# Kernel tuning notes

Hardware: AMD Instinct MI355X
Metric: run time of the kernel (lower is better)

The kernel has to match this reference:

```python
import jax, jax.numpy as jnp
import numpy as np

NEG_INF = -1000000.0  # matches the original's -1e6 masking constant


def setup_inputs() -> dict:
    key = jax.random.key(0)
    ks = jax.random.split(key, 7)
    B, S, A, Q, D = 32, 2048, 1024, 1024, 1024  # batch, src len, attend_dim, query_dim, att_dim
    return {
        "input": jax.random.normal(ks[0], (B, 1, Q), dtype=jnp.float32),
        "context": jax.random.normal(ks[1], (B, S, A), dtype=jnp.float32),
        "W_pre": jax.random.normal(ks[2], (D, A), dtype=jnp.float32) * 0.02,
        "b_pre": jax.random.normal(ks[3], (D,), dtype=jnp.float32) * 0.02,
        "W_q": jax.random.normal(ks[4], (D, Q), dtype=jnp.float32) * 0.02,
        "v": jax.random.normal(ks[5], (D,), dtype=jnp.float32) * 0.02,
        "mask": jax.random.randint(ks[6], (B, 1, S), 0, 2, dtype=jnp.int32),
    }


def reference(input, context, W_pre, b_pre, W_q, v, mask):
    # precompute = linear_pre(context): [B, S, D]
    precompute = jnp.einsum("bsa,da->bsd", context, W_pre) + b_pre
    # targetT = linear_q(input): [B, 1, D]; repeat over S via broadcast
    targetT = jnp.einsum("bqc,dc->bqd", input, W_q)
    tmp = jnp.tanh(precompute + targetT)                 # [B, S, D]
    energy = jnp.einsum("bsd,d->bs", tmp, v)             # linear_v -> [B, S]
    # mask: positions where mask == 0 get -1e6 (energy*(1-m) + m*(-1e6), m = (mask==0))
    masked_out = (mask[:, 0, :] == 0)
    energy = jnp.where(masked_out, NEG_INF, energy)
    score = jax.nn.softmax(energy, axis=1)               # softmax over S
    score_m = score[:, None, :]                          # [B, 1, S]
    weightedContext = jnp.einsum("bqs,bsa->bqa", score_m, context)  # [B, 1, A]
    return weightedContext, score_m, precompute
```

## Files before the change

kernel.cpp:

```cpp
#include <hip/hip_runtime.h>

#define NEG_INF_VAL -1000000.0f

typedef short s16x8 __attribute__((ext_vector_type(8)));
typedef float f32x4 __attribute__((ext_vector_type(4)));

__device__ __forceinline__ unsigned int bf16_rne(float f) {
  unsigned int u = __float_as_uint(f);
  return (u + 0x7fffu + ((u >> 16) & 1u)) >> 16;
}
__device__ __forceinline__ unsigned int pack_bf2(float a, float b) {
  return bf16_rne(a) | (bf16_rne(b) << 16);
}

__device__ __forceinline__ float fast_tanh(float x) {
  float t = __expf(2.f * x);
  return 1.f - __fdividef(2.f, t + 1.f);
}

__global__ __launch_bounds__(256) void convert_bf16_kernel(
    const float* __restrict__ src, unsigned short* __restrict__ dst, long n) {
  long i = ((long)blockIdx.x * blockDim.x + threadIdx.x) * 8;
  long stride = (long)gridDim.x * blockDim.x * 8;
  for (; i < n; i += stride) {
    float4 f0 = *(const float4*)(src + i);
    float4 f1 = *(const float4*)(src + i + 4);
    uint4 o;
    o.x = pack_bf2(f0.x, f0.y);
    o.y = pack_bf2(f0.z, f0.w);
    o.z = pack_bf2(f1.x, f1.y);
    o.w = pack_bf2(f1.z, f1.w);
    *(uint4*)(dst + i) = o;
  }
}

__global__ __launch_bounds__(256) void targetT_kernel(
    const float* __restrict__ input, const float* __restrict__ Wq,
    float* __restrict__ tT) {
  int d0 = blockIdx.x * 8;
  int t = threadIdx.x;
  int b = t >> 3, dl = t & 7;
  __shared__ float in_s[32][32];
  __shared__ float wq_s[8][32];
  float acc = 0.f;
  for (int q0 = 0; q0 < 1024; q0 += 32) {
    int r = t >> 3, c = (t & 7) * 4;
    *(float4*)&in_s[r][c] = *(const float4*)&input[r * 1024 + q0 + c];
    wq_s[t >> 5][t & 31] = Wq[(long)(d0 + (t >> 5)) * 1024 + q0 + (t & 31)];
    __syncthreads();
#pragma unroll
    for (int qq = 0; qq < 32; ++qq)
      acc += in_s[b][qq] * wq_s[dl][qq];
    __syncthreads();
  }
  tT[b * 1024 + d0 + dl] = acc;
}

__device__ __forceinline__ void load_lds16(const void* g, void* l) {
  __builtin_amdgcn_global_load_lds(
      (const __attribute__((address_space(1))) void*)g,
      (__attribute__((address_space(3))) void*)l, 16, 0, 0);
}

__global__ __launch_bounds__(256, 4) void gemm_energy_kernel(
    const unsigned short* __restrict__ A,
    const unsigned short* __restrict__ B,
    const float* __restrict__ b_pre,
    const float* __restrict__ tT,
    const float* __restrict__ vvec,
    float* __restrict__ Cout,
    float* __restrict__ epart) {
  const int K = 1024;
  const int N = 1024;
  int lin = blockIdx.x;
  int w = (lin & 7) * 512 + (lin >> 3);
  int nt = w & 7;
  int mt = w >> 3;
  int m0 = mt * 128, n0 = nt * 128;
  int tid = threadIdx.x;
  int lane = tid & 63, wid = tid >> 6;
  int wr = wid >> 1, wc = wid & 1;

  __shared__ unsigned short sA[128][32];
  __shared__ unsigned short sB[128][32];

  f32x4 acc[4][4] = {};

  int srow = lane >> 2;
  int scol = ((lane & 3) ^ ((lane >> 3) & 3)) * 8;
  const unsigned short* Ag = A + (long)(m0 + wid * 32 + srow) * K + scol;
  const unsigned short* Bg = B + (long)(n0 + wid * 32 + srow) * K + scol;
  unsigned short* sA0 = &sA[wid * 32][0];
  unsigned short* sA1 = &sA[wid * 32 + 16][0];
  unsigned short* sB0 = &sB[wid * 32][0];
  unsigned short* sB1 = &sB[wid * 32 + 16][0];

  int r = lane & 15, g = lane >> 4;
  int slotA = (g ^ ((r >> 1) & 3)) * 8;

  for (int k0 = 0; k0 < K; k0 += 32) {
    load_lds16(Ag, sA0);
    load_lds16(Ag + 16 * K, sA1);
    load_lds16(Bg, sB0);
    load_lds16(Bg + 16 * K, sB1);
    Ag += 32; Bg += 32;
    asm volatile("s_waitcnt vmcnt(0)" ::: "memory");
    __syncthreads();
    s16x8 af[4], bfr[4];
#pragma unroll
    for (int i = 0; i < 4; ++i)
      af[i] = *(const s16x8*)&sA[wr * 64 + i * 16 + r][slotA];
#pragma unroll
    for (int j = 0; j < 4; ++j)
      bfr[j] = *(const s16x8*)&sB[wc * 64 + j * 16 + r][slotA];
    __builtin_amdgcn_s_setprio(1);
#pragma unroll
    for (int i = 0; i < 4; ++i)
#pragma unroll
      for (int j = 0; j < 4; ++j)
        acc[i][j] = __builtin_amdgcn_mfma_f32_16x16x32_bf16(af[i], bfr[j], acc[i][j], 0, 0, 0);
    __builtin_amdgcn_s_setprio(0);
    __syncthreads();
  }

  int b = m0 >> 11;
  float bp[4], tv[4], vv[4];
#pragma unroll
  for (int j = 0; j < 4; ++j) {
    int d = n0 + wc * 64 + j * 16 + r;
    bp[j] = b_pre[d];
    tv[j] = tT[b * 1024 + d];
    vv[j] = vvec[d];
  }
#pragma unroll
  for (int i = 0; i < 4; ++i) {
#pragma unroll
    for (int q = 0; q < 4; ++q) {
      int m = m0 + wr * 64 + i * 16 + g * 4 + q;
      float e = 0.f;
#pragma unroll
      for (int j = 0; j < 4; ++j) {
        float val = acc[i][j][q] + bp[j];
        Cout[(long)m * N + n0 + wc * 64 + j * 16 + r] = val;
        e += fast_tanh(val + tv[j]) * vv[j];
      }
      e += __shfl_xor(e, 1);
      e += __shfl_xor(e, 2);
      e += __shfl_xor(e, 4);
      e += __shfl_xor(e, 8);
      if (r == 0) epart[(long)m * 16 + nt * 2 + wc] = e;
    }
  }
}

__global__ __launch_bounds__(256) void softmax_kernel(
    const float* __restrict__ epart, const int* __restrict__ mask,
    float* __restrict__ score) {
  int b = blockIdx.x;
  int t = threadIdx.x;
  __shared__ float red[256];
  float ev[8];
  float mx = -3.4e38f;
#pragma unroll
  for (int ii = 0; ii < 8; ++ii) {
    int s = ii * 256 + t;
    long m = (long)b * 2048 + s;
    const float4* p = (const float4*)(epart + m * 16);
    float4 p0 = p[0], p1 = p[1], p2 = p[2], p3 = p[3];
    float e = p0.x + p0.y + p0.z + p0.w + p1.x + p1.y + p1.z + p1.w
            + p2.x + p2.y + p2.z + p2.w + p3.x + p3.y + p3.z + p3.w;
    if (mask[b * 2048 + s] == 0) e = NEG_INF_VAL;
    ev[ii] = e;
    mx = fmaxf(mx, e);
  }
  red[t] = mx; __syncthreads();
  for (int off = 128; off > 0; off >>= 1) {
    if (t < off) red[t] = fmaxf(red[t], red[t + off]);
    __syncthreads();
  }
  mx = red[0];
  __syncthreads();
  float sum = 0.f;
#pragma unroll
  for (int ii = 0; ii < 8; ++ii) { ev[ii] = __expf(ev[ii] - mx); sum += ev[ii]; }
  red[t] = sum; __syncthreads();
  for (int off = 128; off > 0; off >>= 1) {
    if (t < off) red[t] += red[t + off];
    __syncthreads();
  }
  float inv = 1.f / red[0];
#pragma unroll
  for (int ii = 0; ii < 8; ++ii)
    score[b * 2048 + ii * 256 + t] = ev[ii] * inv;
}

__global__ __launch_bounds__(256) void wc_partial_kernel(
    const unsigned short* __restrict__ ctx, const float* __restrict__ score,
    float* __restrict__ part) {
  int b = blockIdx.x, sc = blockIdx.y;
  int t = threadIdx.x;
  __shared__ float ssc[64];
  if (t < 64) ssc[t] = score[b * 2048 + sc * 64 + t];
  __syncthreads();
  float acc0 = 0.f, acc1 = 0.f, acc2 = 0.f, acc3 = 0.f;
  const unsigned short* cp = ctx + ((long)b * 2048 + sc * 64) * 1024 + t * 4;
  for (int s = 0; s < 64; ++s) {
    uint2 pk = *(const uint2*)cp;
    cp += 1024;
    float wgt = ssc[s];
    acc0 += wgt * __uint_as_float(pk.x << 16);
    acc1 += wgt * __uint_as_float(pk.x & 0xffff0000u);
    acc2 += wgt * __uint_as_float(pk.y << 16);
    acc3 += wgt * __uint_as_float(pk.y & 0xffff0000u);
  }
  float* pp = part + ((long)(b * 32 + sc)) * 1024 + t * 4;
  pp[0] = acc0; pp[1] = acc1; pp[2] = acc2; pp[3] = acc3;
}

__global__ __launch_bounds__(256) void wc_reduce_kernel(
    const float* __restrict__ part, float* __restrict__ wc) {
  int id = blockIdx.x * 256 + threadIdx.x;
  int b = id >> 10, a = id & 1023;
  float s = 0.f;
#pragma unroll
  for (int scn = 0; scn < 32; ++scn)
    s += part[((long)(b * 32 + scn)) * 1024 + a];
  wc[id] = s;
}

extern "C" void kernel_launch(void* const* d_in, const int* in_sizes, int n_in,
                              void* d_out, int out_size, void* d_ws, size_t ws_size,
                              hipStream_t stream) {
  const float* input   = (const float*)d_in[0];
  const float* context = (const float*)d_in[1];
  const float* W_pre   = (const float*)d_in[2];
  const float* b_pre   = (const float*)d_in[3];
  const float* W_q     = (const float*)d_in[4];
  const float* v       = (const float*)d_in[5];
  const int*   mask    = (const int*)d_in[6];

  float* out       = (float*)d_out;
  float* out_wc    = out;
  float* out_score = out + 32768;
  float* out_pre   = out + 98304;

  const size_t OFF_CTX   = 0;
  const size_t OFF_WPRE  = 134217728;
  const size_t OFF_TT    = 136314880;
  const size_t OFF_EPART = 136445952;
  const size_t OFF_WCP   = 140640256;
  const size_t WS_NEED   = 144834560;
  if (ws_size < WS_NEED) return;

  char* ws = (char*)d_ws;
  unsigned short* ctx_bf  = (unsigned short*)(ws + OFF_CTX);
  unsigned short* wpre_bf = (unsigned short*)(ws + OFF_WPRE);
  float* tT     = (float*)(ws + OFF_TT);
  float* epart  = (float*)(ws + OFF_EPART);
  float* wcpart = (float*)(ws + OFF_WCP);

  convert_bf16_kernel<<<2048, 256, 0, stream>>>(context, ctx_bf, 64LL * 1024 * 1024);
  convert_bf16_kernel<<<256, 256, 0, stream>>>(W_pre, wpre_bf, 1024LL * 1024);
  targetT_kernel<<<128, 256, 0, stream>>>(input, W_q, tT);
  gemm_energy_kernel<<<4096, 256, 0, stream>>>(ctx_bf, wpre_bf, b_pre, tT, v,
                                               out_pre, epart);
  softmax_kernel<<<32, 256, 0, stream>>>(epart, mask, out_score);
  dim3 g5(32, 32);
  wc_partial_kernel<<<g5, 256, 0, stream>>>(ctx_bf, out_score, wcpart);
  wc_reduce_kernel<<<128, 256, 0, stream>>>(wcpart, out_wc);
}
```

Before: 364.7 us.

## Double-buffer GEMM LDS tiles with prefetch and one barrier per phase

Restructures the bf16 GEMM main loop into a software pipeline. Two LDS buffers are used: the tile for a future k-step is issued with global_load_lds while MFMAs run on the current one, and vmcnt is partially waited with a single s_barrier per phase. This replaces the old load, wait-all, sync, compute, sync sequence, which exposed global memory latency on every k-step. It doubles LDS use and lowers the launch-bounds occupancy hint from 4 to 2. The final iteration also prefetches a tile past the end of K that is never used, which reads slightly beyond the row and possibly beyond the buffer.

```diff
diff --git a/kernel.cpp b/kernel.cpp
--- a/kernel.cpp
+++ b/kernel.cpp
@@ -62,16 +62,55 @@
       (__attribute__((address_space(3))) void*)l, 16, 0, 0);
 }
 
-__global__ __launch_bounds__(256, 4) void gemm_energy_kernel(
+#define STAGE_AB(SB, SKK, SKT)                                                       \
+  {                                                                                  \
+    const unsigned short* gpA = Ag + (SKT) * 64 + (SKK) * 32;                        \
+    const unsigned short* gpB = Bg + (SKT) * 64 + (SKK) * 32;                        \
+    char* lpA = dstB + (SB) * 32768 + (SKK) * 8192;                                  \
+    load_lds16(gpA, lpA);                                                            \
+    load_lds16(gpA + 16 * 1024, lpA + 1024);                                         \
+    load_lds16(gpB, lpA + 16384);                                                    \
+    load_lds16(gpB + 16 * 1024, lpA + 16384 + 1024);                                 \
+  }
+
+#define MFMA_ROW(I, AF)                                                              \
+  acc[I][0] = __builtin_amdgcn_mfma_f32_16x16x32_bf16(AF, bf0, acc[I][0], 0, 0, 0);  \
+  acc[I][1] = __builtin_amdgcn_mfma_f32_16x16x32_bf16(AF, bf1, acc[I][1], 0, 0, 0);  \
+  acc[I][2] = __builtin_amdgcn_mfma_f32_16x16x32_bf16(AF, bf2, acc[I][2], 0, 0, 0);  \
+  acc[I][3] = __builtin_amdgcn_mfma_f32_16x16x32_bf16(AF, bf3, acc[I][3], 0, 0, 0);
+
+#define PHASE(BUF, KK, SB, SKT)                                                      \
+  {                                                                                  \
+    const unsigned short* pA = (BUF) ? pA1 : pA0;                                    \
+    const unsigned short* pB = (BUF) ? pB1 : pB0;                                    \
+    s16x8 af0 = *(const s16x8*)(pA + (KK)*4096 +    0);                              \
+    s16x8 af1 = *(const s16x8*)(pA + (KK)*4096 +  512);                              \
+    s16x8 af2 = *(const s16x8*)(pA + (KK)*4096 + 1024);                              \
+    s16x8 af3 = *(const s16x8*)(pA + (KK)*4096 + 1536);                              \
+    s16x8 bf0 = *(const s16x8*)(pB + (KK)*4096 +    0);                              \
+    s16x8 bf1 = *(const s16x8*)(pB + (KK)*4096 +  512);                              \
+    s16x8 bf2 = *(const s16x8*)(pB + (KK)*4096 + 1024);                              \
+    s16x8 bf3 = *(const s16x8*)(pB + (KK)*4096 + 1536);                              \
+    STAGE_AB(SB, KK, SKT)                                                            \
+    __builtin_amdgcn_s_setprio(1);                                                   \
+    MFMA_ROW(0, af0)                                                                 \
+    MFMA_ROW(1, af1)                                                                 \
+    MFMA_ROW(2, af2)                                                                 \
+    MFMA_ROW(3, af3)                                                                 \
+    __builtin_amdgcn_s_setprio(0);                                                   \
+    asm volatile("s_waitcnt vmcnt(4)");                                              \
+    __builtin_amdgcn_sched_barrier(0);                                               \
+    __builtin_amdgcn_s_barrier();                                                    \
+  }
+
+__global__ __launch_bounds__(256, 2) void gemm_energy_kernel(
     const unsigned short* __restrict__ A,
-    const unsigned short* __restrict__ B,
+    const unsigned short* __restrict__ Bm,
     const float* __restrict__ b_pre,
     const float* __restrict__ tT,
     const float* __restrict__ vvec,
     float* __restrict__ Cout,
     float* __restrict__ epart) {
-  const int K = 1024;
-  const int N = 1024;
   int lin = blockIdx.x;
   int w = (lin & 7) * 512 + (lin >> 3);
   int nt = w & 7;
@@ -80,55 +119,52 @@
   int tid = threadIdx.x;
   int lane = tid & 63, wid = tid >> 6;
   int wr = wid >> 1, wc = wid & 1;
-
-  __shared__ unsigned short sA[128][32];
-  __shared__ unsigned short sB[128][32];
+  int r = lane & 15, g = lane >> 4;
+
+  __shared__ unsigned short sMem[2 * 2 * 2 * 128 * 32];
 
   f32x4 acc[4][4] = {};
 
-  int srow = lane >> 2;
-  int scol = ((lane & 3) ^ ((lane >> 3) & 3)) * 8;
-  const unsigned short* Ag = A + (long)(m0 + wid * 32 + srow) * K + scol;
-  const unsigned short* Bg = B + (long)(n0 + wid * 32 + srow) * K + scol;
-  unsigned short* sA0 = &sA[wid * 32][0];
-  unsigned short* sA1 = &sA[wid * 32 + 16][0];
-  unsigned short* sB0 = &sB[wid * 32][0];
-  unsigned short* sB1 = &sB[wid * 32 + 16][0];
-
-  int r = lane & 15, g = lane >> 4;
-  int slotA = (g ^ ((r >> 1) & 3)) * 8;
-
-  for (int k0 = 0; k0 < K; k0 += 32) {
-    load_lds16(Ag, sA0);
-    load_lds16(Ag + 16 * K, sA1);
-    load_lds16(Bg, sB0);
-    load_lds16(Bg + 16 * K, sB1);
-    Ag += 32; Bg += 32;
-    asm volatile("s_waitcnt vmcnt(0)" ::: "memory");
-    __syncthreads();
-    s16x8 af[4], bfr[4];
-#pragma unroll
-    for (int i = 0; i < 4; ++i)
-      af[i] = *(const s16x8*)&sA[wr * 64 + i * 16 + r][slotA];
-#pragma unroll
-    for (int j = 0; j < 4; ++j)
-      bfr[j] = *(const s16x8*)&sB[wc * 64 + j * 16 + r][slotA];
-    __builtin_amdgcn_s_setprio(1);
-#pragma unroll
-    for (int i = 0; i < 4; ++i)
-#pragma unroll
-      for (int j = 0; j < 4; ++j)
-        acc[i][j] = __builtin_amdgcn_mfma_f32_16x16x32_bf16(af[i], bfr[j], acc[i][j], 0, 0, 0);
-    __builtin_amdgcn_s_setprio(0);
-    __syncthreads();
-  }
+  int physoff = (g ^ ((r >> 1) & 3)) * 8;
+
+  int aoffe = (wr * 64 + r) * 32 + physoff;
+  int boffe = (wc * 64 + r) * 32 + physoff;
+  const unsigned short* pA0 = sMem + aoffe;
+  const unsigned short* pA1 = sMem + 16384 + aoffe;
+  const unsigned short* pB0 = sMem + 8192 + boffe;
+  const unsigned short* pB1 = sMem + 24576 + boffe;
+  char* dstB = (char*)sMem + wid * 2048;
+
+  int srow = wid * 32 + (lane >> 2);
+  int slog8 = ((lane & 3) ^ ((lane >> 3) & 3)) * 8;
+  const unsigned short* Abase = A + (long)(m0 + srow) * 1024 + slog8;
+  const unsigned short* Bbase = Bm + (long)(n0 + srow) * 1024 + slog8;
+  const unsigned short* Ag = Abase;
+  const unsigned short* Bg = Bbase;
+
+  STAGE_AB(0, 0, 0)
+  STAGE_AB(0, 1, 0)
+  asm volatile("s_waitcnt vmcnt(4)");
+  __builtin_amdgcn_sched_barrier(0);
+  __builtin_amdgcn_s_barrier();
+
+#pragma unroll 1
+  for (int t0 = 0; t0 < 16; t0 += 2) {
+    Ag = Abase + t0 * 64;
+    Bg = Bbase + t0 * 64;
+    PHASE(0, 0,  1, 1)
+    PHASE(0, 1,  1, 1)
+    PHASE(1, 0,  0, 2)
+    PHASE(1, 1,  0, 2)
+  }
+  asm volatile("s_waitcnt vmcnt(0)");
 
   int b = m0 >> 11;
-  float bp[4], tv[4], vv[4];
+  float bias[4], tv[4], vv[4];
 #pragma unroll
   for (int j = 0; j < 4; ++j) {
     int d = n0 + wc * 64 + j * 16 + r;
-    bp[j] = b_pre[d];
+    bias[j] = b_pre[d];
     tv[j] = tT[b * 1024 + d];
     vv[j] = vvec[d];
   }
@@ -140,8 +176,8 @@
       float e = 0.f;
 #pragma unroll
       for (int j = 0; j < 4; ++j) {
-        float val = acc[i][j][q] + bp[j];
-        Cout[(long)m * N + n0 + wc * 64 + j * 16 + r] = val;
+        float val = acc[i][j][q] + bias[j];
+        Cout[(long)m * 1024 + n0 + wc * 64 + j * 16 + r] = val;
         e += fast_tanh(val + tv[j]) * vv[j];
       }
       e += __shfl_xor(e, 1);
```

New measurement: 402.3 us. +10.3%, slower.
